# Kernel optimization log

Measured on AMD Instinct MI355X. Metric: run time of the kernel, lower is better.

Reference implementation:

```python
import jax, jax.numpy as jnp
import numpy as np

NUM_HEADS = 8


def setup_inputs() -> dict:
    key = jax.random.key(0)
    ks = jax.random.split(key, 8)
    B, C, H, W = 8, 512, 64, 64
    s = 1.0 / np.sqrt(C)
    return {
        "guide": jax.random.normal(ks[0], (B, C), dtype=jnp.float32),
        "hidden_rep": jax.random.normal(ks[1], (B, C, H, W), dtype=jnp.float32),
        "Wq": jax.random.normal(ks[2], (C, C), dtype=jnp.float32) * s,
        "bq": jnp.zeros((C,), dtype=jnp.float32),
        "Wk": jax.random.normal(ks[3], (C, C), dtype=jnp.float32) * s,
        "bk": jnp.zeros((C,), dtype=jnp.float32),
        "Wv": jax.random.normal(ks[4], (C, C), dtype=jnp.float32) * s,
        "bv": jnp.zeros((C,), dtype=jnp.float32),
    }


def reference(guide, hidden_rep, Wq, bq, Wk, bk, Wv, bv):
    B, C, H, W = hidden_rep.shape
    nh = NUM_HEADS
    d = C // nh
    scale = 1.0 / (d ** 0.5)

    # hidden_rep: [B,C,H,W] -> [B, HW, C] (token-major, matching torch permute+reshape)
    hr = hidden_rep.transpose(0, 2, 3, 1).reshape(B, H * W, C)

    # guide is broadcast identically over all HW positions in the original;
    # the linear commutes with the broadcast, so compute once then broadcast.
    q_row = guide @ Wq.T + bq                                   # [B, C]
    q_tok = jnp.broadcast_to(q_row[:, None, :], (B, H * W, C))  # [B, HW, C]
    k_tok = hr @ Wk.T + bk                                      # [B, HW, C]
    v_tok = hr @ Wv.T + bv                                      # [B, HW, C]

    # Faithful replication of torch split_heads: view [B,HW,C] as [B,nh,d,H,W]
    # (this scrambles spatial/channel axes exactly as the original does),
    # then permute to [B, nh, H, W, d].
    def split_heads(x):
        return x.reshape(B, nh, d, H, W).transpose(0, 1, 3, 4, 2)

    q = split_heads(q_tok)  # [B, nh, H, W, d]
    k = split_heads(k_tok)
    v = split_heads(v_tok)

    # Row-wise attention: softmax over the width axis only.
    scores = jnp.einsum('bnhqd,bnhkd->bnhqk', q, k) * scale  # [B, nh, H, W, W]
    weights = jax.nn.softmax(scores, axis=-1)
    attended = jnp.einsum('bnhqk,bnhkd->bnhqd', weights, v)  # [B, nh, H, W, d]

    # permute(0,1,4,2,3) -> [B, nh, d, H, W] -> [B, C, H, W]
    return attended.transpose(0, 1, 4, 2, 3).reshape(B, C, H, W)
```

## Files before the change

### kernel.cpp

```cpp
#include <hip/hip_runtime.h>
#include <hip/hip_bf16.h>
#include <stdint.h>


typedef __attribute__((ext_vector_type(8))) short bf16x8_t;
typedef __attribute__((ext_vector_type(4))) float f32x4_t;

__device__ __forceinline__ unsigned short f2bf(float f) {
  unsigned int u = __float_as_uint(f);
  u += 0x7FFFu + ((u >> 16) & 1u);
  return (unsigned short)(u >> 16);
}

__device__ __forceinline__ void gload16(const void* g, void* lds) {
  __builtin_amdgcn_global_load_lds(
      (const __attribute__((address_space(1))) unsigned int*)g,
      (__attribute__((address_space(3))) unsigned int*)lds, 16, 0, 0);
}

__global__ __launch_bounds__(256) void k_trans(const float* __restrict__ hid,
                                               unsigned short* __restrict__ XT,
                                               float* __restrict__ hrsum,
                                               const float* __restrict__ Wv,
                                               unsigned short* __restrict__ Wvb) {
  int bid = blockIdx.x;
  int tid = threadIdx.x;
  if (bid >= 512) {
    int blk = bid - 512;
#pragma unroll
    for (int i = 0; i < 16; ++i) {
      int idx = blk * 4096 + i * 256 + tid;
      float4 v = ((const float4*)Wv)[idx];
      ushort4 o;
      o.x = f2bf(v.x); o.y = f2bf(v.y); o.z = f2bf(v.z); o.w = f2bf(v.w);
      ((ushort4*)Wvb)[idx] = o;
    }
    return;
  }
  int cb = bid & 7, n = (bid >> 3) & 7, b = bid >> 6;
  __shared__ float T[64][65];
  __shared__ float hsred[64][8];

  for (int i = tid; i < 512; i += 256) ((float*)hsred)[i] = 0.f;

  float part[4][4];
#pragma unroll
  for (int m = 0; m < 4; ++m)
#pragma unroll
    for (int i = 0; i < 4; ++i) part[m][i] = 0.f;

  const int f4 = tid & 15;
  const int r0 = tid >> 4;
  const float* srcbase = hid + (size_t)(b * 512 + cb * 64) * 4096 + n * 512;
  unsigned short* xtbase = XT + (size_t)(b * 8 + n) * 512 * 512 + cb * 64;

  for (int jc = 0; jc < 8; ++jc) {
    __syncthreads();
#pragma unroll
    for (int m = 0; m < 4; ++m) {
      int r = r0 + 16 * m;
      float4 v = *(const float4*)(srcbase + (size_t)r * 4096 + jc * 64 + f4 * 4);
      T[r][f4 * 4 + 0] = v.x;  T[r][f4 * 4 + 1] = v.y;
      T[r][f4 * 4 + 2] = v.z;  T[r][f4 * 4 + 3] = v.w;
      part[m][0] += v.x; part[m][1] += v.y; part[m][2] += v.z; part[m][3] += v.w;
    }
    __syncthreads();
#pragma unroll
    for (int p = 0; p < 2; ++p) {
      int jl = (tid >> 3) + p * 32;
      int o = tid & 7;
      unsigned short t0 = f2bf(T[o * 8 + 0][jl]);
      unsigned short t1 = f2bf(T[o * 8 + 1][jl]);
      unsigned short t2 = f2bf(T[o * 8 + 2][jl]);
      unsigned short t3 = f2bf(T[o * 8 + 3][jl]);
      unsigned short t4 = f2bf(T[o * 8 + 4][jl]);
      unsigned short t5 = f2bf(T[o * 8 + 5][jl]);
      unsigned short t6 = f2bf(T[o * 8 + 6][jl]);
      unsigned short t7 = f2bf(T[o * 8 + 7][jl]);
      uint4 pk;
      pk.x = (unsigned)t0 | ((unsigned)t1 << 16);
      pk.y = (unsigned)t2 | ((unsigned)t3 << 16);
      pk.z = (unsigned)t4 | ((unsigned)t5 << 16);
      pk.w = (unsigned)t6 | ((unsigned)t7 << 16);
      *(uint4*)(xtbase + (size_t)(jc * 64 + jl) * 512 + o * 8) = pk;
    }
  }
  __syncthreads();
  {
    int gbase = (tid & 1) * 4;
#pragma unroll
    for (int m = 0; m < 4; ++m) {
      int r = r0 + 16 * m;
#pragma unroll
      for (int i = 0; i < 4; ++i) atomicAdd(&hsred[r][gbase + i], part[m][i]);
    }
  }
  __syncthreads();
  float* hout = hrsum + (size_t)(b * 8 + n) * 8 * 512 + cb * 64;
  for (int i = tid; i < 512; i += 256) {
    int g = i >> 6, r = i & 63;
    hout[(size_t)g * 512 + r] = hsred[r][g];
  }
}

__global__ __launch_bounds__(256) void k_k2(const float* __restrict__ hrsum,
                                            const float* __restrict__ Wk,
                                            const float* __restrict__ bk,
                                            const float* __restrict__ guide,
                                            const float* __restrict__ Wq,
                                            const float* __restrict__ bq,
                                            float* __restrict__ K2,
                                            float* __restrict__ qs) {
  int bid = blockIdx.x;
  int rt = bid >> 4, ct = bid & 15;
  bool isQ = (rt == 16);
  const float* A = isQ ? guide : (hrsum + (size_t)rt * 32 * 512);
  const float* Bm = isQ ? Wq : Wk;
  int arows = isQ ? 8 : 32;
  int tid = threadIdx.x;
  __shared__ float Ah[32][36];
  __shared__ float Bh[32][36];
  int r = tid >> 3, f = tid & 7;
  int oy = (tid >> 4) * 2, ox = (tid & 15) * 2;
  float a00 = 0.f, a01 = 0.f, a10 = 0.f, a11 = 0.f;

  for (int kc = 0; kc < 16; ++kc) {
    __syncthreads();
    float4 av = (r < arows) ? *(const float4*)(A + (size_t)r * 512 + kc * 32 + f * 4)
                            : make_float4(0.f, 0.f, 0.f, 0.f);
    *(float4*)(&Ah[r][f * 4]) = av;
    float4 bv = *(const float4*)(Bm + (size_t)(ct * 32 + r) * 512 + kc * 32 + f * 4);
    *(float4*)(&Bh[r][f * 4]) = bv;
    __syncthreads();
#pragma unroll
    for (int kk = 0; kk < 32; kk += 4) {
      float4 x0 = *(float4*)(&Ah[oy][kk]);
      float4 x1 = *(float4*)(&Ah[oy + 1][kk]);
      float4 y0 = *(float4*)(&Bh[ox][kk]);
      float4 y1 = *(float4*)(&Bh[ox + 1][kk]);
      a00 += x0.x * y0.x + x0.y * y0.y + x0.z * y0.z + x0.w * y0.w;
      a01 += x0.x * y1.x + x0.y * y1.y + x0.z * y1.z + x0.w * y1.w;
      a10 += x1.x * y0.x + x1.y * y0.y + x1.z * y0.z + x1.w * y0.w;
      a11 += x1.x * y1.x + x1.y * y1.y + x1.z * y1.z + x1.w * y1.w;
    }
  }
  int c0 = ct * 32 + ox;
  if (!isQ) {
    int row0 = rt * 32 + oy;
    K2[(size_t)row0 * 512 + c0]           = a00 + 64.f * bk[c0];
    K2[(size_t)row0 * 512 + c0 + 1]       = a01 + 64.f * bk[c0 + 1];
    K2[(size_t)(row0 + 1) * 512 + c0]     = a10 + 64.f * bk[c0];
    K2[(size_t)(row0 + 1) * 512 + c0 + 1] = a11 + 64.f * bk[c0 + 1];
  } else if (oy < 8) {
    const float scale = 0.125f;
    qs[(size_t)oy * 512 + c0]           = (a00 + bq[c0]) * scale;
    qs[(size_t)oy * 512 + c0 + 1]       = (a01 + bq[c0 + 1]) * scale;
    qs[(size_t)(oy + 1) * 512 + c0]     = (a10 + bq[c0]) * scale;
    qs[(size_t)(oy + 1) * 512 + c0 + 1] = (a11 + bq[c0 + 1]) * scale;
  }
}

__global__ __launch_bounds__(512, 4) void k_fused(
    const unsigned short* __restrict__ XT, const unsigned short* __restrict__ Wvb,
    const float* __restrict__ K2, const float* __restrict__ qs,
    const float* __restrict__ bv, float* __restrict__ out) {
  int p = blockIdx.x;
  int xcd = p & 7, idx = p >> 3;
  int slab = xcd * 8 + (idx & 7);
  int g = idx >> 3;
  int n = slab & 7, b = slab >> 3;

  int tid = threadIdx.x;
  int w = tid >> 6, l = tid & 63;
  int l15 = l & 15, l4 = l >> 4, lr = l >> 3, lc = l & 7;

  __shared__ __align__(16) unsigned char smem[81920];
  unsigned char* Vp = smem + 16384 + w * 8192;

  const unsigned swzel = (unsigned)((lc ^ lr) << 3);
  const unsigned short* bsrc = XT + (size_t)slab * 512 * 512;
  const unsigned short* wbase = Wvb + (size_t)(w * 64 + l15) * 512 + l4 * 8;
  const int brow = 8 * (w * 8 + lr) + g;

  float alpha = qs[(size_t)b * 512 + w * 64 + l];
  float beta  = K2[(size_t)(slab * 8 + g) * 512 + w * 64 + l];
  float bvreg = bv[w * 64 + l];

  gload16(bsrc + (size_t)brow * 512 + 0 * 64 + swzel, smem + 0 * 8192 + w * 1024);
  gload16(bsrc + (size_t)brow * 512 + 1 * 64 + swzel, smem + 1 * 8192 + w * 1024);

  bf16x8_t af[2][4];
#pragma unroll
  for (int mt = 0; mt < 4; ++mt)
    af[0][mt] = *(const bf16x8_t*)(wbase + mt * 16 * 512);

  f32x4_t acc[4][4];
#pragma unroll
  for (int i = 0; i < 4; ++i)
#pragma unroll
    for (int j = 0; j < 4; ++j) acc[i][j] = (f32x4_t){0.f, 0.f, 0.f, 0.f};

#pragma unroll
  for (int kc = 0; kc < 8; ++kc) {
    if (kc < 7) asm volatile("s_waitcnt vmcnt(5)" ::: "memory");
    else        asm volatile("s_waitcnt vmcnt(4)" ::: "memory");
    __builtin_amdgcn_s_barrier();
    asm volatile("" ::: "memory");
    unsigned char* Bb = smem + (kc & 1) * 8192;
#pragma unroll
    for (int ks = 0; ks < 2; ++ks) {
      const int s = kc * 2 + ks;
      if (s < 15) {
#pragma unroll
        for (int mt = 0; mt < 4; ++mt)
          af[(s + 1) & 1][mt] =
              *(const bf16x8_t*)(wbase + mt * 16 * 512 + (s + 1) * 32);
      }
      bf16x8_t bfr[4];
#pragma unroll
      for (int nt = 0; nt < 4; ++nt) {
        unsigned row = (unsigned)(nt * 16 + l15);
        bfr[nt] = *(const bf16x8_t*)(Bb + row * 128 +
                                     ((unsigned)(ks * 64 + l4 * 16) ^ ((row & 7) << 4)));
      }
      __builtin_amdgcn_s_setprio(1);
#pragma unroll
      for (int mt = 0; mt < 4; ++mt)
#pragma unroll
        for (int nt = 0; nt < 4; ++nt)
          acc[mt][nt] = __builtin_amdgcn_mfma_f32_16x16x32_bf16(
              af[s & 1][mt], bfr[nt], acc[mt][nt], 0, 0, 0);
      __builtin_amdgcn_s_setprio(0);
    }
    asm volatile("" ::: "memory");
    __builtin_amdgcn_s_barrier();
    asm volatile("" ::: "memory");
    if (kc < 6)
      gload16(bsrc + (size_t)brow * 512 + (kc + 2) * 64 + swzel,
              smem + (kc & 1) * 8192 + w * 1024);
  }

#pragma unroll
  for (int mt = 0; mt < 4; ++mt) {
    float bq0 = __shfl(bvreg, mt * 16 + l4 * 4 + 0);
    float bq1 = __shfl(bvreg, mt * 16 + l4 * 4 + 1);
    float bq2 = __shfl(bvreg, mt * 16 + l4 * 4 + 2);
    float bq3 = __shfl(bvreg, mt * 16 + l4 * 4 + 3);
#pragma unroll
    for (int nt = 0; nt < 4; ++nt) {
      unsigned dd = (unsigned)(nt * 16 + l15);
      uint2 pk;
      pk.x = (unsigned)f2bf(acc[mt][nt][0] + bq0) |
             ((unsigned)f2bf(acc[mt][nt][1] + bq1) << 16);
      pk.y = (unsigned)f2bf(acc[mt][nt][2] + bq2) |
             ((unsigned)f2bf(acc[mt][nt][3] + bq3) << 16);
      *(uint2*)(Vp + dd * 128 +
                ((unsigned)(mt * 32 + l4 * 8) ^ ((dd & 7) << 4))) = pk;
    }
  }

  float bmax = beta, bmin = beta;
#pragma unroll
  for (int o = 32; o >= 1; o >>= 1) {
    bmax = fmaxf(bmax, __shfl_xor(bmax, o));
    bmin = fminf(bmin, __shfl_xor(bmin, o));
  }
  float m = alpha >= 0.f ? alpha * bmax : alpha * bmin;
  float ssum = 0.f;
#pragma unroll 8
  for (int kk = 0; kk < 64; ++kk)
    ssum += __expf(fmaf(alpha, __shfl(beta, kk), -m));
  float inv = 1.0f / ssum;

  f32x4_t acc2[4][4];
#pragma unroll
  for (int i = 0; i < 4; ++i)
#pragma unroll
    for (int j = 0; j < 4; ++j) acc2[i][j] = (f32x4_t){0.f, 0.f, 0.f, 0.f};

#pragma unroll
  for (int ks = 0; ks < 2; ++ks) {
    bf16x8_t va[4];
#pragma unroll
    for (int mt = 0; mt < 4; ++mt) {
      unsigned dd = (unsigned)(mt * 16 + l15);
      va[mt] = *(const bf16x8_t*)(Vp + dd * 128 +
                ((unsigned)(ks * 64 + l4 * 16) ^ ((dd & 7) << 4)));
    }
    float bvv[8];
#pragma unroll
    for (int i = 0; i < 8; ++i) bvv[i] = __shfl(beta, ks * 32 + l4 * 8 + i);
    bf16x8_t pb[4];
#pragma unroll
    for (int nt = 0; nt < 4; ++nt) {
      int qq = nt * 16 + l15;
      float aq = __shfl(alpha, qq);
      float mq = __shfl(m, qq);
      float iq = __shfl(inv, qq);
      bf16x8_t pp;
#pragma unroll
      for (int i = 0; i < 8; ++i)
        pp[i] = (short)f2bf(__expf(fmaf(aq, bvv[i], -mq)) * iq);
      pb[nt] = pp;
    }
#pragma unroll
    for (int mt = 0; mt < 4; ++mt)
#pragma unroll
      for (int nt = 0; nt < 4; ++nt)
        acc2[mt][nt] = __builtin_amdgcn_mfma_f32_16x16x32_bf16(
            va[mt], pb[nt], acc2[mt][nt], 0, 0, 0);
  }

#pragma unroll
  for (int mt = 0; mt < 4; ++mt) {
#pragma unroll
    for (int r = 0; r < 4; ++r) {
      int dd = mt * 16 + l4 * 4 + r;
      size_t base = (((size_t)(b * 512 + n * 64 + dd)) * 64 + (g * 8 + w)) * 64;
#pragma unroll
      for (int nt = 0; nt < 4; ++nt)
        out[base + nt * 16 + l15] = acc2[mt][nt][r];
    }
  }
}

extern "C" void kernel_launch(void* const* d_in, const int* in_sizes, int n_in,
                              void* d_out, int out_size, void* d_ws, size_t ws_size,
                              hipStream_t stream) {
  const float* guide = (const float*)d_in[0];
  const float* hid   = (const float*)d_in[1];
  const float* Wq    = (const float*)d_in[2];
  const float* bq    = (const float*)d_in[3];
  const float* Wk    = (const float*)d_in[4];
  const float* bk    = (const float*)d_in[5];
  const float* Wv    = (const float*)d_in[6];
  const float* bv    = (const float*)d_in[7];
  float* out = (float*)d_out;

  char* ws = (char*)d_ws;
  unsigned short* XT  = (unsigned short*)(ws);
  unsigned short* Wvb = (unsigned short*)(ws + 33554432);
  float* hrsum        = (float*)(ws + 34078720);
  float* K2           = (float*)(ws + 35127296);
  float* qs           = (float*)(ws + 36175872);

  k_trans<<<528, 256, 0, stream>>>(hid, XT, hrsum, Wv, Wvb);
  k_k2<<<272, 256, 0, stream>>>(hrsum, Wk, bk, guide, Wq, bq, K2, qs);
  k_fused<<<512, 512, 0, stream>>>(XT, Wvb, K2, qs, bv, out);
}
```

Measured before the change: 95.63 us.

## Load full X slab up front, pass V through shuffles, swap MFMA operands for vector stores

The kernel now issues all eight B-tile loads into a 64KB LDS buffer at once, replacing the double-buffered pipeline with its per-step barriers. The V tile no longer goes through LDS: the bf16-packed accumulators are exchanged between lanes with shuffles to form the second MFMA operand. The second GEMM's operands are swapped so each lane writes float4 output stores. The cost is more register pressure from pk[4][4] plus many shuffles, and the upfront load exposes global latency with no overlap against compute.

After: 101.8 us. +6.4%, slower.

```diff
diff --git a/kernel.cpp b/kernel.cpp
--- a/kernel.cpp
+++ b/kernel.cpp
@@ -174,72 +174,61 @@
   int w = tid >> 6, l = tid & 63;
   int l15 = l & 15, l4 = l >> 4, lr = l >> 3, lc = l & 7;
 
-  __shared__ __align__(16) unsigned char smem[81920];
-  unsigned char* Vp = smem + 16384 + w * 8192;
+  __shared__ __align__(16) unsigned char smem[65536];
 
   const unsigned swzel = (unsigned)((lc ^ lr) << 3);
   const unsigned short* bsrc = XT + (size_t)slab * 512 * 512;
   const unsigned short* wbase = Wvb + (size_t)(w * 64 + l15) * 512 + l4 * 8;
   const int brow = 8 * (w * 8 + lr) + g;
 
+#pragma unroll
+  for (int i = 0; i < 8; ++i)
+    gload16(bsrc + (size_t)brow * 512 + i * 64 + swzel, smem + i * 8192 + w * 1024);
+
   float alpha = qs[(size_t)b * 512 + w * 64 + l];
   float beta  = K2[(size_t)(slab * 8 + g) * 512 + w * 64 + l];
   float bvreg = bv[w * 64 + l];
 
-  gload16(bsrc + (size_t)brow * 512 + 0 * 64 + swzel, smem + 0 * 8192 + w * 1024);
-  gload16(bsrc + (size_t)brow * 512 + 1 * 64 + swzel, smem + 1 * 8192 + w * 1024);
+  f32x4_t acc[4][4];
+#pragma unroll
+  for (int i = 0; i < 4; ++i)
+#pragma unroll
+    for (int j = 0; j < 4; ++j) acc[i][j] = (f32x4_t){0.f, 0.f, 0.f, 0.f};
+
+  __syncthreads();
 
   bf16x8_t af[2][4];
 #pragma unroll
   for (int mt = 0; mt < 4; ++mt)
     af[0][mt] = *(const bf16x8_t*)(wbase + mt * 16 * 512);
 
-  f32x4_t acc[4][4];
-#pragma unroll
-  for (int i = 0; i < 4; ++i)
-#pragma unroll
-    for (int j = 0; j < 4; ++j) acc[i][j] = (f32x4_t){0.f, 0.f, 0.f, 0.f};
-
-#pragma unroll
-  for (int kc = 0; kc < 8; ++kc) {
-    if (kc < 7) asm volatile("s_waitcnt vmcnt(5)" ::: "memory");
-    else        asm volatile("s_waitcnt vmcnt(4)" ::: "memory");
-    __builtin_amdgcn_s_barrier();
-    asm volatile("" ::: "memory");
-    unsigned char* Bb = smem + (kc & 1) * 8192;
-#pragma unroll
-    for (int ks = 0; ks < 2; ++ks) {
-      const int s = kc * 2 + ks;
-      if (s < 15) {
-#pragma unroll
-        for (int mt = 0; mt < 4; ++mt)
-          af[(s + 1) & 1][mt] =
-              *(const bf16x8_t*)(wbase + mt * 16 * 512 + (s + 1) * 32);
-      }
-      bf16x8_t bfr[4];
-#pragma unroll
-      for (int nt = 0; nt < 4; ++nt) {
-        unsigned row = (unsigned)(nt * 16 + l15);
-        bfr[nt] = *(const bf16x8_t*)(Bb + row * 128 +
-                                     ((unsigned)(ks * 64 + l4 * 16) ^ ((row & 7) << 4)));
-      }
-      __builtin_amdgcn_s_setprio(1);
+#pragma unroll
+  for (int s = 0; s < 16; ++s) {
+    if (s < 15) {
 #pragma unroll
       for (int mt = 0; mt < 4; ++mt)
-#pragma unroll
-        for (int nt = 0; nt < 4; ++nt)
-          acc[mt][nt] = __builtin_amdgcn_mfma_f32_16x16x32_bf16(
-              af[s & 1][mt], bfr[nt], acc[mt][nt], 0, 0, 0);
-      __builtin_amdgcn_s_setprio(0);
-    }
-    asm volatile("" ::: "memory");
-    __builtin_amdgcn_s_barrier();
-    asm volatile("" ::: "memory");
-    if (kc < 6)
-      gload16(bsrc + (size_t)brow * 512 + (kc + 2) * 64 + swzel,
-              smem + (kc & 1) * 8192 + w * 1024);
-  }
-
+        af[(s + 1) & 1][mt] =
+            *(const bf16x8_t*)(wbase + mt * 16 * 512 + (s + 1) * 32);
+    }
+    unsigned char* Bb = smem + (s >> 1) * 8192;
+    bf16x8_t bfr[4];
+#pragma unroll
+    for (int nt = 0; nt < 4; ++nt) {
+      unsigned row = (unsigned)(nt * 16 + l15);
+      bfr[nt] = *(const bf16x8_t*)(Bb + row * 128 +
+                ((unsigned)((s & 1) * 64 + l4 * 16) ^ ((row & 7) << 4)));
+    }
+    __builtin_amdgcn_s_setprio(1);
+#pragma unroll
+    for (int mt = 0; mt < 4; ++mt)
+#pragma unroll
+      for (int nt = 0; nt < 4; ++nt)
+        acc[mt][nt] = __builtin_amdgcn_mfma_f32_16x16x32_bf16(
+            af[s & 1][mt], bfr[nt], acc[mt][nt], 0, 0, 0);
+    __builtin_amdgcn_s_setprio(0);
+  }
+
+  uint2 pk[4][4];
 #pragma unroll
   for (int mt = 0; mt < 4; ++mt) {
     float bq0 = __shfl(bvreg, mt * 16 + l4 * 4 + 0);
@@ -248,14 +237,10 @@
     float bq3 = __shfl(bvreg, mt * 16 + l4 * 4 + 3);
 #pragma unroll
     for (int nt = 0; nt < 4; ++nt) {
-      unsigned dd = (unsigned)(nt * 16 + l15);
-      uint2 pk;
-      pk.x = (unsigned)f2bf(acc[mt][nt][0] + bq0) |
-             ((unsigned)f2bf(acc[mt][nt][1] + bq1) << 16);
-      pk.y = (unsigned)f2bf(acc[mt][nt][2] + bq2) |
-             ((unsigned)f2bf(acc[mt][nt][3] + bq3) << 16);
-      *(uint2*)(Vp + dd * 128 +
-                ((unsigned)(mt * 32 + l4 * 8) ^ ((dd & 7) << 4))) = pk;
+      pk[mt][nt].x = (unsigned)f2bf(acc[mt][nt][0] + bq0) |
+                     ((unsigned)f2bf(acc[mt][nt][1] + bq1) << 16);
+      pk[mt][nt].y = (unsigned)f2bf(acc[mt][nt][2] + bq2) |
+                     ((unsigned)f2bf(acc[mt][nt][3] + bq3) << 16);
     }
   }
 
@@ -278,48 +263,59 @@
 #pragma unroll
     for (int j = 0; j < 4; ++j) acc2[i][j] = (f32x4_t){0.f, 0.f, 0.f, 0.f};
 
+  const int sib0 = (l4 & 1) * 32 + l15;
+  const int sib1 = sib0 + 16;
+  const bool hi = (l4 >= 2);
+
 #pragma unroll
   for (int ks = 0; ks < 2; ++ks) {
-    bf16x8_t va[4];
-#pragma unroll
-    for (int mt = 0; mt < 4; ++mt) {
-      unsigned dd = (unsigned)(mt * 16 + l15);
-      va[mt] = *(const bf16x8_t*)(Vp + dd * 128 +
-                ((unsigned)(ks * 64 + l4 * 16) ^ ((dd & 7) << 4)));
-    }
-    float bvv[8];
-#pragma unroll
-    for (int i = 0; i < 8; ++i) bvv[i] = __shfl(beta, ks * 32 + l4 * 8 + i);
-    bf16x8_t pb[4];
-#pragma unroll
-    for (int nt = 0; nt < 4; ++nt) {
-      int qq = nt * 16 + l15;
-      float aq = __shfl(alpha, qq);
-      float mq = __shfl(m, qq);
-      float iq = __shfl(inv, qq);
+    bf16x8_t pa[4];
+    float bb[8];
+#pragma unroll
+    for (int i = 0; i < 8; ++i) bb[i] = __shfl(beta, ks * 32 + l4 * 8 + i);
+#pragma unroll
+    for (int mt2 = 0; mt2 < 4; ++mt2) {
+      float aq = __shfl(alpha, mt2 * 16 + l15);
+      float mq = __shfl(m, mt2 * 16 + l15);
+      float iq = __shfl(inv, mt2 * 16 + l15);
       bf16x8_t pp;
 #pragma unroll
       for (int i = 0; i < 8; ++i)
-        pp[i] = (short)f2bf(__expf(fmaf(aq, bvv[i], -mq)) * iq);
-      pb[nt] = pp;
-    }
-#pragma unroll
-    for (int mt = 0; mt < 4; ++mt)
-#pragma unroll
-      for (int nt = 0; nt < 4; ++nt)
-        acc2[mt][nt] = __builtin_amdgcn_mfma_f32_16x16x32_bf16(
-            va[mt], pb[nt], acc2[mt][nt], 0, 0, 0);
-  }
-
-#pragma unroll
-  for (int mt = 0; mt < 4; ++mt) {
-#pragma unroll
-    for (int r = 0; r < 4; ++r) {
-      int dd = mt * 16 + l4 * 4 + r;
-      size_t base = (((size_t)(b * 512 + n * 64 + dd)) * 64 + (g * 8 + w)) * 64;
-#pragma unroll
-      for (int nt = 0; nt < 4; ++nt)
-        out[base + nt * 16 + l15] = acc2[mt][nt][r];
+        pp[i] = (short)f2bf(__expf(fmaf(aq, bb[i], -mq)) * iq);
+      pa[mt2] = pp;
+    }
+    bf16x8_t vb[4];
+#pragma unroll
+    for (int nt2 = 0; nt2 < 4; ++nt2) {
+      unsigned lo_x0 = __shfl(pk[ks * 2][nt2].x, sib0);
+      unsigned lo_y0 = __shfl(pk[ks * 2][nt2].y, sib0);
+      unsigned lo_x1 = __shfl(pk[ks * 2][nt2].x, sib1);
+      unsigned lo_y1 = __shfl(pk[ks * 2][nt2].y, sib1);
+      unsigned hi_x0 = __shfl(pk[ks * 2 + 1][nt2].x, sib0);
+      unsigned hi_y0 = __shfl(pk[ks * 2 + 1][nt2].y, sib0);
+      unsigned hi_x1 = __shfl(pk[ks * 2 + 1][nt2].x, sib1);
+      unsigned hi_y1 = __shfl(pk[ks * 2 + 1][nt2].y, sib1);
+      uint4 q = make_uint4(hi ? hi_x0 : lo_x0, hi ? hi_y0 : lo_y0,
+                           hi ? hi_x1 : lo_x1, hi ? hi_y1 : lo_y1);
+      vb[nt2] = *(const bf16x8_t*)&q;
+    }
+#pragma unroll
+    for (int mt2 = 0; mt2 < 4; ++mt2)
+#pragma unroll
+      for (int nt2 = 0; nt2 < 4; ++nt2)
+        acc2[mt2][nt2] = __builtin_amdgcn_mfma_f32_16x16x32_bf16(
+            pa[mt2], vb[nt2], acc2[mt2][nt2], 0, 0, 0);
+  }
+
+#pragma unroll
+  for (int nt2 = 0; nt2 < 4; ++nt2) {
+    int dd = nt2 * 16 + l15;
+    size_t base = (((size_t)(b * 512 + n * 64 + dd)) * 64 + (g * 8 + w)) * 64;
+#pragma unroll
+    for (int mt2 = 0; mt2 < 4; ++mt2) {
+      float4 v = make_float4(acc2[mt2][nt2][0], acc2[mt2][nt2][1],
+                             acc2[mt2][nt2][2], acc2[mt2][nt2][3]);
+      *(float4*)(out + base + mt2 * 16 + l4 * 4) = v;
     }
   }
 }
```

## Split transpose blocks in half, prefetch loads, and preload whole B slab in fused kernel

Applied to the files above, without the earlier changes.

The transpose kernel now gives each block half the channel rows, which doubles the grid. It register-prefetches the next chunk's float4 loads while the current chunk is written to LDS. The fused kernel drops its double-buffered K loop: all eight B chunks are loaded into 64KB of LDS up front behind one barrier, and the V staging area reuses that same LDS. This removes per-chunk barriers and the software pipeline, but it loses the overlap of loads with MFMA work and the register prefetch of the A fragments.

Result: no change. 94.70 us (-1.0%).

```diff
diff --git a/kernel.cpp b/kernel.cpp
--- a/kernel.cpp
+++ b/kernel.cpp
@@ -25,8 +25,8 @@
                                                unsigned short* __restrict__ Wvb) {
   int bid = blockIdx.x;
   int tid = threadIdx.x;
-  if (bid >= 512) {
-    int blk = bid - 512;
+  if (bid >= 1024) {
+    int blk = bid - 1024;
 #pragma unroll
     for (int i = 0; i < 16; ++i) {
       int idx = blk * 4096 + i * 256 + tid;
@@ -37,68 +37,88 @@
     }
     return;
   }
-  int cb = bid & 7, n = (bid >> 3) & 7, b = bid >> 6;
-  __shared__ float T[64][65];
-  __shared__ float hsred[64][8];
-
-  for (int i = tid; i < 512; i += 256) ((float*)hsred)[i] = 0.f;
-
-  float part[4][4];
-#pragma unroll
-  for (int m = 0; m < 4; ++m)
+  int rh = bid & 1, cb = (bid >> 1) & 7, n = (bid >> 4) & 7, b = bid >> 7;
+  __shared__ float T[32][65];
+  __shared__ float hsred[32][8];
+  ((float*)hsred)[tid] = 0.f;
+
+  float part[2][4];
+#pragma unroll
+  for (int m = 0; m < 2; ++m)
 #pragma unroll
     for (int i = 0; i < 4; ++i) part[m][i] = 0.f;
 
   const int f4 = tid & 15;
   const int r0 = tid >> 4;
-  const float* srcbase = hid + (size_t)(b * 512 + cb * 64) * 4096 + n * 512;
-  unsigned short* xtbase = XT + (size_t)(b * 8 + n) * 512 * 512 + cb * 64;
-
-  for (int jc = 0; jc < 8; ++jc) {
-    __syncthreads();
-#pragma unroll
-    for (int m = 0; m < 4; ++m) {
+  const float* srcbase = hid + (size_t)(b * 512 + cb * 64 + rh * 32) * 4096 + n * 512;
+  unsigned short* xtbase =
+      XT + (size_t)(b * 8 + n) * 512 * 512 + cb * 64 + rh * 32;
+
+  float4 va[2], vb2[2];
+#pragma unroll
+  for (int m = 0; m < 2; ++m)
+    va[m] = *(const float4*)(srcbase + (size_t)(r0 + 16 * m) * 4096 + f4 * 4);
+
+#define TSTEP(JC, CUR, NXT, LAST)                                              \
+  do {                                                                         \
+    _Pragma("unroll")                                                          \
+    for (int m_ = 0; m_ < 2; ++m_) {                                           \
+      int r_ = r0 + 16 * m_;                                                   \
+      T[r_][f4 * 4 + 0] = CUR[m_].x;  T[r_][f4 * 4 + 1] = CUR[m_].y;           \
+      T[r_][f4 * 4 + 2] = CUR[m_].z;  T[r_][f4 * 4 + 3] = CUR[m_].w;           \
+      part[m_][0] += CUR[m_].x; part[m_][1] += CUR[m_].y;                      \
+      part[m_][2] += CUR[m_].z; part[m_][3] += CUR[m_].w;                      \
+    }                                                                          \
+    if (!(LAST)) {                                                             \
+      _Pragma("unroll")                                                        \
+      for (int m_ = 0; m_ < 2; ++m_)                                           \
+        NXT[m_] = *(const float4*)(srcbase + (size_t)(r0 + 16 * m_) * 4096 +   \
+                                   ((JC) + 1) * 64 + f4 * 4);                  \
+    }                                                                          \
+    __syncthreads();                                                           \
+    {                                                                          \
+      int jl_ = tid >> 2, o_ = tid & 3;                                        \
+      unsigned short t0 = f2bf(T[o_ * 8 + 0][jl_]);                            \
+      unsigned short t1 = f2bf(T[o_ * 8 + 1][jl_]);                            \
+      unsigned short t2 = f2bf(T[o_ * 8 + 2][jl_]);                            \
+      unsigned short t3 = f2bf(T[o_ * 8 + 3][jl_]);                            \
+      unsigned short t4 = f2bf(T[o_ * 8 + 4][jl_]);                            \
+      unsigned short t5 = f2bf(T[o_ * 8 + 5][jl_]);                            \
+      unsigned short t6 = f2bf(T[o_ * 8 + 6][jl_]);                            \
+      unsigned short t7 = f2bf(T[o_ * 8 + 7][jl_]);                            \
+      uint4 pk_;                                                               \
+      pk_.x = (unsigned)t0 | ((unsigned)t1 << 16);                             \
+      pk_.y = (unsigned)t2 | ((unsigned)t3 << 16);                             \
+      pk_.z = (unsigned)t4 | ((unsigned)t5 << 16);                             \
+      pk_.w = (unsigned)t6 | ((unsigned)t7 << 16);                             \
+      *(uint4*)(xtbase + (size_t)((JC) * 64 + jl_) * 512 + o_ * 8) = pk_;      \
+    }                                                                          \
+    __syncthreads();                                                           \
+  } while (0)
+
+  TSTEP(0, va, vb2, 0);
+  TSTEP(1, vb2, va, 0);
+  TSTEP(2, va, vb2, 0);
+  TSTEP(3, vb2, va, 0);
+  TSTEP(4, va, vb2, 0);
+  TSTEP(5, vb2, va, 0);
+  TSTEP(6, va, vb2, 0);
+  TSTEP(7, vb2, va, 1);
+#undef TSTEP
+
+  {
+    int gbase = (f4 & 1) * 4;
+#pragma unroll
+    for (int m = 0; m < 2; ++m) {
       int r = r0 + 16 * m;
-      float4 v = *(const float4*)(srcbase + (size_t)r * 4096 + jc * 64 + f4 * 4);
-      T[r][f4 * 4 + 0] = v.x;  T[r][f4 * 4 + 1] = v.y;
-      T[r][f4 * 4 + 2] = v.z;  T[r][f4 * 4 + 3] = v.w;
-      part[m][0] += v.x; part[m][1] += v.y; part[m][2] += v.z; part[m][3] += v.w;
-    }
-    __syncthreads();
-#pragma unroll
-    for (int p = 0; p < 2; ++p) {
-      int jl = (tid >> 3) + p * 32;
-      int o = tid & 7;
-      unsigned short t0 = f2bf(T[o * 8 + 0][jl]);
-      unsigned short t1 = f2bf(T[o * 8 + 1][jl]);
-      unsigned short t2 = f2bf(T[o * 8 + 2][jl]);
-      unsigned short t3 = f2bf(T[o * 8 + 3][jl]);
-      unsigned short t4 = f2bf(T[o * 8 + 4][jl]);
-      unsigned short t5 = f2bf(T[o * 8 + 5][jl]);
-      unsigned short t6 = f2bf(T[o * 8 + 6][jl]);
-      unsigned short t7 = f2bf(T[o * 8 + 7][jl]);
-      uint4 pk;
-      pk.x = (unsigned)t0 | ((unsigned)t1 << 16);
-      pk.y = (unsigned)t2 | ((unsigned)t3 << 16);
-      pk.z = (unsigned)t4 | ((unsigned)t5 << 16);
-      pk.w = (unsigned)t6 | ((unsigned)t7 << 16);
-      *(uint4*)(xtbase + (size_t)(jc * 64 + jl) * 512 + o * 8) = pk;
+#pragma unroll
+      for (int i = 0; i < 4; ++i) atomicAdd(&hsred[r][gbase + i], part[m][i]);
     }
   }
   __syncthreads();
+  float* hout = hrsum + (size_t)(b * 8 + n) * 4096 + cb * 64 + rh * 32;
   {
-    int gbase = (tid & 1) * 4;
-#pragma unroll
-    for (int m = 0; m < 4; ++m) {
-      int r = r0 + 16 * m;
-#pragma unroll
-      for (int i = 0; i < 4; ++i) atomicAdd(&hsred[r][gbase + i], part[m][i]);
-    }
-  }
-  __syncthreads();
-  float* hout = hrsum + (size_t)(b * 8 + n) * 8 * 512 + cb * 64;
-  for (int i = tid; i < 512; i += 256) {
-    int g = i >> 6, r = i & 63;
+    int g = tid >> 5, r = tid & 31;
     hout[(size_t)g * 512 + r] = hsred[r][g];
   }
 }
@@ -174,72 +194,56 @@
   int w = tid >> 6, l = tid & 63;
   int l15 = l & 15, l4 = l >> 4, lr = l >> 3, lc = l & 7;
 
-  __shared__ __align__(16) unsigned char smem[81920];
-  unsigned char* Vp = smem + 16384 + w * 8192;
+  __shared__ __align__(16) unsigned char smem[65536];
 
   const unsigned swzel = (unsigned)((lc ^ lr) << 3);
   const unsigned short* bsrc = XT + (size_t)slab * 512 * 512;
   const unsigned short* wbase = Wvb + (size_t)(w * 64 + l15) * 512 + l4 * 8;
   const int brow = 8 * (w * 8 + lr) + g;
 
+#pragma unroll
+  for (int i = 0; i < 8; ++i)
+    gload16(bsrc + (size_t)brow * 512 + i * 64 + swzel, smem + i * 8192 + w * 1024);
+
   float alpha = qs[(size_t)b * 512 + w * 64 + l];
   float beta  = K2[(size_t)(slab * 8 + g) * 512 + w * 64 + l];
   float bvreg = bv[w * 64 + l];
 
-  gload16(bsrc + (size_t)brow * 512 + 0 * 64 + swzel, smem + 0 * 8192 + w * 1024);
-  gload16(bsrc + (size_t)brow * 512 + 1 * 64 + swzel, smem + 1 * 8192 + w * 1024);
-
-  bf16x8_t af[2][4];
-#pragma unroll
-  for (int mt = 0; mt < 4; ++mt)
-    af[0][mt] = *(const bf16x8_t*)(wbase + mt * 16 * 512);
-
   f32x4_t acc[4][4];
 #pragma unroll
   for (int i = 0; i < 4; ++i)
 #pragma unroll
     for (int j = 0; j < 4; ++j) acc[i][j] = (f32x4_t){0.f, 0.f, 0.f, 0.f};
 
-#pragma unroll
-  for (int kc = 0; kc < 8; ++kc) {
-    if (kc < 7) asm volatile("s_waitcnt vmcnt(5)" ::: "memory");
-    else        asm volatile("s_waitcnt vmcnt(4)" ::: "memory");
-    __builtin_amdgcn_s_barrier();
-    asm volatile("" ::: "memory");
-    unsigned char* Bb = smem + (kc & 1) * 8192;
-#pragma unroll
-    for (int ks = 0; ks < 2; ++ks) {
-      const int s = kc * 2 + ks;
-      if (s < 15) {
-#pragma unroll
-        for (int mt = 0; mt < 4; ++mt)
-          af[(s + 1) & 1][mt] =
-              *(const bf16x8_t*)(wbase + mt * 16 * 512 + (s + 1) * 32);
-      }
-      bf16x8_t bfr[4];
-#pragma unroll
-      for (int nt = 0; nt < 4; ++nt) {
-        unsigned row = (unsigned)(nt * 16 + l15);
-        bfr[nt] = *(const bf16x8_t*)(Bb + row * 128 +
-                                     ((unsigned)(ks * 64 + l4 * 16) ^ ((row & 7) << 4)));
-      }
-      __builtin_amdgcn_s_setprio(1);
-#pragma unroll
-      for (int mt = 0; mt < 4; ++mt)
-#pragma unroll
-        for (int nt = 0; nt < 4; ++nt)
-          acc[mt][nt] = __builtin_amdgcn_mfma_f32_16x16x32_bf16(
-              af[s & 1][mt], bfr[nt], acc[mt][nt], 0, 0, 0);
-      __builtin_amdgcn_s_setprio(0);
-    }
-    asm volatile("" ::: "memory");
-    __builtin_amdgcn_s_barrier();
-    asm volatile("" ::: "memory");
-    if (kc < 6)
-      gload16(bsrc + (size_t)brow * 512 + (kc + 2) * 64 + swzel,
-              smem + (kc & 1) * 8192 + w * 1024);
-  }
-
+  __syncthreads();
+
+#pragma unroll
+  for (int s = 0; s < 16; ++s) {
+    bf16x8_t af[4];
+#pragma unroll
+    for (int mt = 0; mt < 4; ++mt)
+      af[mt] = *(const bf16x8_t*)(wbase + mt * 16 * 512 + s * 32);
+    unsigned char* Bb = smem + (s >> 1) * 8192;
+    bf16x8_t bfr[4];
+#pragma unroll
+    for (int nt = 0; nt < 4; ++nt) {
+      unsigned row = (unsigned)(nt * 16 + l15);
+      bfr[nt] = *(const bf16x8_t*)(Bb + row * 128 +
+                ((unsigned)((s & 1) * 64 + l4 * 16) ^ ((row & 7) << 4)));
+    }
+    __builtin_amdgcn_s_setprio(1);
+#pragma unroll
+    for (int mt = 0; mt < 4; ++mt)
+#pragma unroll
+      for (int nt = 0; nt < 4; ++nt)
+        acc[mt][nt] = __builtin_amdgcn_mfma_f32_16x16x32_bf16(
+            af[mt], bfr[nt], acc[mt][nt], 0, 0, 0);
+    __builtin_amdgcn_s_setprio(0);
+  }
+
+  __syncthreads();
+
+  unsigned char* Vp = smem + w * 8192;
 #pragma unroll
   for (int mt = 0; mt < 4; ++mt) {
     float bq0 = __shfl(bvreg, mt * 16 + l4 * 4 + 0);
@@ -344,7 +348,7 @@
   float* K2           = (float*)(ws + 35127296);
   float* qs           = (float*)(ws + 36175872);
 
-  k_trans<<<528, 256, 0, stream>>>(hid, XT, hrsum, Wv, Wvb);
+  k_trans<<<1040, 256, 0, stream>>>(hid, XT, hrsum, Wv, Wvb);
   k_k2<<<272, 256, 0, stream>>>(hrsum, Wk, bk, guide, Wq, bq, K2, qs);
   k_fused<<<512, 512, 0, stream>>>(XT, Wvb, K2, qs, bv, out);
 }
```
